# Kernel optimization log

Hardware: AMD Instinct MI355X
Metric: run time of the kernel (lower is better)

The kernel has to match this reference:

```python
import jax, jax.numpy as jnp
import numpy as np

L = 4096
D = 150  # TRANSITION_STATE_OUTPUTS_DIM


def setup_inputs() -> dict:
    key = jax.random.key(0)
    k1, k2 = jax.random.split(key)
    adj = jax.random.uniform(k1, (L, L, 2), dtype=jnp.float32)
    h = jax.random.normal(k2, (L, D), dtype=jnp.float32)
    return {"unpreprocessed_unweight_adj_matrix": adj, "h": h}


def reference(unpreprocessed_unweight_adj_matrix, h):
    # Original math: h_in[j,d]  = sum_{i,e} adj[i,j,e] * h[i,d]
    #                h_out[i,d] = sum_{j,e} adj[i,j,e] * h[j,d]
    # Contract the 2 edge types first, then a single [L,L]x[L,D] matmul each way,
    # avoiding the O(L^2 * 2 * D) broadcasted intermediate of the original.
    n, d = h.shape
    A = unpreprocessed_unweight_adj_matrix.reshape(n, n, 2).sum(axis=2)  # [L, L]
    h_in = A.T @ h   # sum over source nodes i -> [L, D]
    h_out = A @ h    # sum over target nodes j -> [L, D]
    return (h_in, h_out)
```

## Files before the change

### kernel.cpp

```cpp
#include <hip/hip_runtime.h>

#define LN 4096
#define DN 150
#define NT 10
#define KSPLIT 4
#define KQ 1024
#define NSS 4

typedef __attribute__((ext_vector_type(8))) short bf16x8;
typedef __attribute__((ext_vector_type(4))) float f32x4;

__device__ __forceinline__ unsigned short f2bf(float f) {
    unsigned int u = __builtin_bit_cast(unsigned int, f);
    u = (u + 0x7FFFu + ((u >> 16) & 1u)) >> 16;
    return (unsigned short)u;
}

__global__ __launch_bounds__(256) void k_zero(f32x4* __restrict__ p, int n4) {
    int i = blockIdx.x * 256 + threadIdx.x;
    if (i < n4) p[i] = (f32x4){0.f, 0.f, 0.f, 0.f};
}

__global__ __launch_bounds__(256) void k_transpose(const float* __restrict__ h,
                                                   unsigned short* __restrict__ Ht) {
    __shared__ float S[64][33];
    const int i0 = blockIdx.x * 64;
    const int d0 = blockIdx.y * 32;
    const int tid = threadIdx.x;
    for (int t = tid; t < 64 * 32; t += 256) {
        int ii = t >> 5, dd = t & 31;
        int d = d0 + dd;
        S[ii][dd] = (d < DN) ? h[(size_t)(i0 + ii) * DN + d] : 0.0f;
    }
    __syncthreads();
    for (int t = tid; t < 32 * 64; t += 256) {
        int dd = t >> 6, ii = t & 63;
        Ht[(size_t)(d0 + dd) * LN + i0 + ii] = f2bf(S[ii][dd]);
    }
}

__global__ __launch_bounds__(256) void k_reduce(const float* __restrict__ pIn,
                                                const float* __restrict__ pOut,
                                                float* __restrict__ out, int n4) {
    int i = blockIdx.x * 256 + threadIdx.x;
    if (i >= n4) return;
    const f32x4* a = reinterpret_cast<const f32x4*>(pIn);
    const f32x4* b = reinterpret_cast<const f32x4*>(pOut);
    f32x4 s0 = a[i], s1 = b[i];
    #pragma unroll
    for (int k = 1; k < KSPLIT; ++k) {
        s0 += a[(size_t)k * n4 + i];
        s1 += b[(size_t)k * n4 + i];
    }
    reinterpret_cast<f32x4*>(out)[i] = s0;
    reinterpret_cast<f32x4*>(out)[n4 + i] = s1;
}

template <int TR>
__global__ __launch_bounds__(256, 2) void k_gemm(const float* __restrict__ adj,
                                                 const unsigned short* __restrict__ Ht,
                                                 float* __restrict__ part,
                                                 float* __restrict__ out) {
    __shared__ unsigned short At[2][32 * 256];
    __shared__ float red[32][160];
    const int tid  = threadIdx.x;
    const int lane = tid & 63;
    const int wave = tid >> 6;
    const int r16  = lane & 15;
    const int g    = lane >> 4;
    const int m0 = blockIdx.x * 32;
    const int kq = blockIdx.y * KQ;

    f32x4 acc[2][NT];
    #pragma unroll
    for (int mt = 0; mt < 2; ++mt)
        #pragma unroll
        for (int n = 0; n < NT; ++n) acc[mt][n] = (f32x4){0.f, 0.f, 0.f, 0.f};

    f32x4 sv[16];

    auto stage_load = [&](int ss) {
        if (TR == 0) {
            const int row = tid >> 7;
            const int kk  = tid & 127;
            #pragma unroll
            for (int rr = 0; rr < 16; ++rr) {
                int rowr = rr * 2 + row;
                sv[rr] = *reinterpret_cast<const f32x4*>(
                    adj + ((size_t)(m0 + rowr) * LN + kq + ss * 256 + 2 * kk) * 2);
            }
        } else {
            const int iof = tid >> 4;
            const int jp  = tid & 15;
            #pragma unroll
            for (int rr = 0; rr < 16; ++rr) {
                int il = rr * 16 + iof;
                sv[rr] = *reinterpret_cast<const f32x4*>(
                    adj + ((size_t)(kq + ss * 256 + il) * LN + m0 + jp * 2) * 2);
            }
        }
    };
    auto stage_write = [&](int buf) {
        if (TR == 0) {
            const int row = tid >> 7;
            const int kk  = tid & 127;
            #pragma unroll
            for (int rr = 0; rr < 16; ++rr) {
                int rowr = rr * 2 + row;
                unsigned int u = (unsigned int)f2bf(sv[rr].x + sv[rr].y) |
                                 ((unsigned int)f2bf(sv[rr].z + sv[rr].w) << 16);
                *reinterpret_cast<unsigned int*>(
                    &At[buf][rowr * 256 + ((2 * kk) ^ ((rowr & 15) << 3))]) = u;
            }
        } else {
            const int iof = tid >> 4;
            const int jA  = (tid & 15) * 2, jB = jA + 1;
            #pragma unroll
            for (int rr = 0; rr < 16; ++rr) {
                int k = rr * 16 + iof;
                At[buf][jA * 256 + (k ^ ((jA & 15) << 3))] = f2bf(sv[rr].x + sv[rr].y);
                At[buf][jB * 256 + (k ^ ((jB & 15) << 3))] = f2bf(sv[rr].z + sv[rr].w);
            }
        }
    };
    auto frag = [&](int buf, int mt, int s) {
        int row  = mt * 16 + r16;
        int kloc = wave * 64 + s * 32 + g * 8;
        return *reinterpret_cast<const bf16x8*>(&At[buf][row * 256 + (kloc ^ (r16 << 3))]);
    };
    auto loadB = [&](bf16x8 (&bb)[NT], int ss, int s) {
        int k = kq + ss * 256 + wave * 64 + s * 32 + g * 8;
        #pragma unroll
        for (int n = 0; n < NT; ++n)
            bb[n] = *reinterpret_cast<const bf16x8*>(Ht + (size_t)(n * 16 + r16) * LN + k);
    };

    stage_load(0);
    stage_write(0);
    __syncthreads();
    for (int ss = 0; ss < NSS; ++ss) {
        const int buf = ss & 1;
        if (ss + 1 < NSS) stage_load(ss + 1);
        #pragma unroll
        for (int s = 0; s < 2; ++s) {
            bf16x8 B[NT];
            loadB(B, ss, s);
            bf16x8 a0 = frag(buf, 0, s);
            bf16x8 a1 = frag(buf, 1, s);
            #pragma unroll
            for (int n = 0; n < NT; ++n) {
                acc[0][n] = __builtin_amdgcn_mfma_f32_16x16x32_bf16(a0, B[n], acc[0][n], 0, 0, 0);
                acc[1][n] = __builtin_amdgcn_mfma_f32_16x16x32_bf16(a1, B[n], acc[1][n], 0, 0, 0);
            }
        }
        __syncthreads();
        if (ss + 1 < NSS) stage_write(buf ^ 1);
        __syncthreads();
    }

    for (int w4 = 0; w4 < 4; ++w4) {
        if (wave == w4) {
            #pragma unroll
            for (int mt = 0; mt < 2; ++mt)
                #pragma unroll
                for (int n = 0; n < NT; ++n)
                    #pragma unroll
                    for (int q = 0; q < 4; ++q) {
                        int row = mt * 16 + g * 4 + q;
                        if (w4 == 0) red[row][n * 16 + r16]  = acc[mt][n][q];
                        else         red[row][n * 16 + r16] += acc[mt][n][q];
                    }
        }
        __syncthreads();
    }
    if (part) {
        float* dst = part + (size_t)blockIdx.y * (LN * DN);
        for (int t2 = tid; t2 < 32 * DN; t2 += 256) {
            int row = t2 / DN, col = t2 % DN;
            dst[(size_t)(m0 + row) * DN + col] = red[row][col];
        }
    } else {
        for (int t2 = tid; t2 < 32 * DN; t2 += 256) {
            int row = t2 / DN, col = t2 % DN;
            atomicAdd(&out[(size_t)(m0 + row) * DN + col], red[row][col]);
        }
    }
}

extern "C" void kernel_launch(void* const* d_in, const int* in_sizes, int n_in,
                              void* d_out, int out_size, void* d_ws, size_t ws_size,
                              hipStream_t stream) {
    const float* adj = (const float*)d_in[0];
    const float* h   = (const float*)d_in[1];
    float* out = (float*)d_out;
    char* ws = (char*)d_ws;

    unsigned short* Ht = (unsigned short*)ws;
    const size_t offPin  = 2u << 20;
    const size_t psz     = (size_t)KSPLIT * LN * DN * 4;
    const size_t offPout = offPin + psz;
    const size_t need    = offPout + psz;

    k_transpose<<<dim3(64, 5), 256, 0, stream>>>(h, Ht);

    if (ws_size >= need) {
        float* pIn  = (float*)(ws + offPin);
        float* pOut = (float*)(ws + offPout);
        k_gemm<0><<<dim3(128, KSPLIT), 256, 0, stream>>>(adj, Ht, pOut, nullptr);
        k_gemm<1><<<dim3(128, KSPLIT), 256, 0, stream>>>(adj, Ht, pIn,  nullptr);
        const int n4 = (LN * DN) / 4;
        k_reduce<<<(n4 + 255) / 256, 256, 0, stream>>>(pIn, pOut, out, n4);
    } else {
        const int n4 = out_size / 4;
        k_zero<<<(n4 + 255) / 256, 256, 0, stream>>>((f32x4*)out, n4);
        k_gemm<0><<<dim3(128, KSPLIT), 256, 0, stream>>>(adj, Ht, nullptr, out + (size_t)LN * DN);
        k_gemm<1><<<dim3(128, KSPLIT), 256, 0, stream>>>(adj, Ht, nullptr, out);
    }
}
```

Measured before the change: 100.1 us.

## Add dedicated A@h GEMM kernel with direct global-to-LDS loads and 8-way K split

Replaces the non-transposed GEMM path with a new kernel that streams fp32 adjacency rows straight into LDS using global_load_lds. The edge-sum and bf16 conversion move to fragment read time instead of a register staging pass. It uses 64-row tiles with one M tile per wave, a swizzled LDS layout and a finer 8-way K split. The goal is to cut register staging and LDS write cost on the largest memory stream. In exchange it needs more partial-sum workspace and a larger reduce, and it converts from LDS repeatedly.

```diff
diff --git a/kernel.cpp b/kernel.cpp
--- a/kernel.cpp
+++ b/kernel.cpp
@@ -3,12 +3,19 @@
 #define LN 4096
 #define DN 150
 #define NT 10
+
 #define KSPLIT 4
 #define KQ 1024
 #define NSS 4
 
+#define KS0 8
+#define KQ0 (LN / KS0)
+#define NS0 (KQ0 / 64)
+
 typedef __attribute__((ext_vector_type(8))) short bf16x8;
 typedef __attribute__((ext_vector_type(4))) float f32x4;
+typedef __attribute__((address_space(1))) const unsigned char gl_u8;
+typedef __attribute__((address_space(3))) unsigned char lds_u8;
 
 __device__ __forceinline__ unsigned short f2bf(float f) {
     unsigned int u = __builtin_bit_cast(unsigned int, f);
@@ -48,12 +55,85 @@
     const f32x4* b = reinterpret_cast<const f32x4*>(pOut);
     f32x4 s0 = a[i], s1 = b[i];
     #pragma unroll
-    for (int k = 1; k < KSPLIT; ++k) {
-        s0 += a[(size_t)k * n4 + i];
-        s1 += b[(size_t)k * n4 + i];
-    }
+    for (int k = 1; k < KSPLIT; ++k) s0 += a[(size_t)k * n4 + i];
+    #pragma unroll
+    for (int k = 1; k < KS0; ++k)    s1 += b[(size_t)k * n4 + i];
     reinterpret_cast<f32x4*>(out)[i] = s0;
     reinterpret_cast<f32x4*>(out)[n4 + i] = s1;
+}
+
+__global__ __launch_bounds__(256, 2) void k_gemm_a(const float* __restrict__ adj,
+                                                   const unsigned short* __restrict__ Ht,
+                                                   float* __restrict__ part) {
+    __shared__ char At[2][32768];
+    const int tid  = threadIdx.x;
+    const int lane = tid & 63;
+    const int w    = tid >> 6;
+    const int r16  = lane & 15;
+    const int g    = lane >> 4;
+    const int m0 = blockIdx.x * 64;
+    const int kq = blockIdx.y * KQ0;
+
+    f32x4 acc[NT];
+    #pragma unroll
+    for (int n = 0; n < NT; ++n) acc[n] = (f32x4){0.f, 0.f, 0.f, 0.f};
+
+    auto stage = [&](int buf, int ss) {
+        const int kb = kq + ss * 64;
+        #pragma unroll
+        for (int t = 0; t < 8; ++t) {
+            const int r0  = w * 16 + t * 2;
+            const int row = r0 + (lane >> 5);
+            const float* src = adj + ((size_t)(m0 + row) * LN + kb) * 2
+                                   + (((lane & 31) ^ (row & 7)) << 2);
+            __builtin_amdgcn_global_load_lds((gl_u8*)src,
+                                             (lds_u8*)(&At[buf][r0 * 512]), 16, 0, 0);
+        }
+    };
+
+    const int rA  = w * 16 + r16;
+    const int swz = rA & 7;
+
+    stage(0, 0);
+    __syncthreads();
+    for (int ss = 0; ss < NS0; ++ss) {
+        const int buf = ss & 1;
+        if (ss + 1 < NS0) stage(buf ^ 1, ss + 1);
+        #pragma unroll
+        for (int sh = 0; sh < 2; ++sh) {
+            const int k = kq + ss * 64 + sh * 32 + g * 8;
+            bf16x8 B[NT];
+            #pragma unroll
+            for (int n = 0; n < NT; ++n)
+                B[n] = *reinterpret_cast<const bf16x8*>(Ht + (size_t)(n * 16 + r16) * LN + k);
+            f32x4 v[4];
+            #pragma unroll
+            for (int j = 0; j < 4; ++j)
+                v[j] = *reinterpret_cast<const f32x4*>(
+                    &At[buf][rA * 512 + (((sh * 16 + g * 4 + j) ^ swz) << 4)]);
+            bf16x8 a;
+            #pragma unroll
+            for (int j = 0; j < 4; ++j) {
+                a[2 * j]     = (short)f2bf(v[j].x + v[j].y);
+                a[2 * j + 1] = (short)f2bf(v[j].z + v[j].w);
+            }
+            #pragma unroll
+            for (int n = 0; n < NT; ++n)
+                acc[n] = __builtin_amdgcn_mfma_f32_16x16x32_bf16(a, B[n], acc[n], 0, 0, 0);
+        }
+        __syncthreads();
+    }
+
+    float* dst = part + (size_t)blockIdx.y * (LN * DN);
+    #pragma unroll
+    for (int n = 0; n < NT; ++n) {
+        #pragma unroll
+        for (int q = 0; q < 4; ++q) {
+            int row = w * 16 + g * 4 + q;
+            int col = n * 16 + r16;
+            if (col < DN) dst[(size_t)(m0 + row) * DN + col] = acc[n][q];
+        }
+    }
 }
 
 template <int TR>
@@ -197,17 +277,16 @@
 
     unsigned short* Ht = (unsigned short*)ws;
     const size_t offPin  = 2u << 20;
-    const size_t psz     = (size_t)KSPLIT * LN * DN * 4;
-    const size_t offPout = offPin + psz;
-    const size_t need    = offPout + psz;
+    const size_t offPout = offPin + (size_t)KSPLIT * LN * DN * 4;
+    const size_t need    = offPout + (size_t)KS0 * LN * DN * 4;
 
     k_transpose<<<dim3(64, 5), 256, 0, stream>>>(h, Ht);
 
     if (ws_size >= need) {
         float* pIn  = (float*)(ws + offPin);
         float* pOut = (float*)(ws + offPout);
-        k_gemm<0><<<dim3(128, KSPLIT), 256, 0, stream>>>(adj, Ht, pOut, nullptr);
-        k_gemm<1><<<dim3(128, KSPLIT), 256, 0, stream>>>(adj, Ht, pIn,  nullptr);
+        k_gemm_a<<<dim3(64, KS0), 256, 0, stream>>>(adj, Ht, pOut);
+        k_gemm<1><<<dim3(128, KSPLIT), 256, 0, stream>>>(adj, Ht, pIn, nullptr);
         const int n4 = (LN * DN) / 4;
         k_reduce<<<(n4 + 255) / 256, 256, 0, stream>>>(pIn, pOut, out, n4);
     } else {
```

New measurement: 108.7 us. +8.5%, slower.
